# Kernel optimization log

Measured on AMD Instinct MI355X. Metric: run time of the kernel, lower is better.

The kernel has to match this reference:

```python
import jax, jax.numpy as jnp
import numpy as np
from jax import lax

H = 64  # hidden_size

def _lstm_layer(x, w_ih, w_hh, b_ih, b_hh):
    # x: (B, T, in). PyTorch gate order [i, f, g, o]; gates = x@W_ih^T + h@W_hh^T + b_ih + b_hh.
    B, T, _ = x.shape
    xw = jnp.einsum('bti,gi->btg', x, w_ih) + (b_ih + b_hh)  # (B, T, 4H), input projection hoisted out of scan

    def step(carry, xw_t):
        h, c = carry
        gates = xw_t + h @ w_hh.T                     # (B, 4H)
        i, f, g, o = jnp.split(gates, 4, axis=-1)
        i = jax.nn.sigmoid(i)
        f = jax.nn.sigmoid(f)
        g = jnp.tanh(g)
        o = jax.nn.sigmoid(o)
        c = f * c + i * g
        h = o * jnp.tanh(c)
        return (h, c), h

    h0 = jnp.zeros((B, H), dtype=x.dtype)
    c0 = jnp.zeros((B, H), dtype=x.dtype)
    (h_n, _), hs = lax.scan(step, (h0, c0), jnp.swapaxes(xw, 0, 1))  # hs: (T, B, H)
    return jnp.swapaxes(hs, 0, 1), h_n


def setup_inputs() -> dict:
    key = jax.random.key(0)
    ks = jax.random.split(key, 12)
    s = 1.0 / np.sqrt(H)  # PyTorch LSTM init scale
    return {
        'x':     jax.random.normal(ks[0], (2048, 512, 4), dtype=jnp.float32),
        'w_ih0': jax.random.uniform(ks[1], (4 * H, 4), jnp.float32, -s, s),
        'w_hh0': jax.random.uniform(ks[2], (4 * H, H), jnp.float32, -s, s),
        'b_ih0': jax.random.uniform(ks[3], (4 * H,), jnp.float32, -s, s),
        'b_hh0': jax.random.uniform(ks[4], (4 * H,), jnp.float32, -s, s),
        'w_ih1': jax.random.uniform(ks[5], (4 * H, H), jnp.float32, -s, s),
        'w_hh1': jax.random.uniform(ks[6], (4 * H, H), jnp.float32, -s, s),
        'b_ih1': jax.random.uniform(ks[7], (4 * H,), jnp.float32, -s, s),
        'b_hh1': jax.random.uniform(ks[8], (4 * H,), jnp.float32, -s, s),
        'fc_w':  jax.random.uniform(ks[9], (H, H), jnp.float32, -s, s),
        'fc_b':  jax.random.uniform(ks[10], (H,), jnp.float32, -s, s),
    }


def reference(x, w_ih0, w_hh0, b_ih0, b_hh0, w_ih1, w_hh1, b_ih1, b_hh1, fc_w, fc_b):
    # 2-layer LSTM (eval mode: inter-layer dropout inactive), take last layer's final hidden,
    # then Linear + tanh.
    h1_seq, _ = _lstm_layer(x, w_ih0, w_hh0, b_ih0, b_hh0)
    _, h_n = _lstm_layer(h1_seq, w_ih1, w_hh1, b_ih1, b_hh1)
    return jnp.tanh(h_n @ fc_w.T + fc_b)
```

## Files before the change

### kernel.cpp

```cpp
#include <hip/hip_runtime.h>


#define HID 64
#define TSTEPS 512
#define MB 8
#define BLK 512
#define HSTR 88
#define LOG2E  1.4426950408889634f
#define LOG2E2 2.8853900817779268f

typedef _Float16 f16;
typedef _Float16 half8 __attribute__((ext_vector_type(8)));
typedef _Float16 half4 __attribute__((ext_vector_type(4)));
typedef float f32x4 __attribute__((ext_vector_type(4)));

__device__ __forceinline__ float tanh2(float y) {
    return fmaf(2.0f, __builtin_amdgcn_rcpf(1.0f + __builtin_amdgcn_exp2f(-y)), -1.0f);
}

__global__ __launch_bounds__(BLK, 2) void lstm_mfma(
    const float* __restrict__ x,
    const float* __restrict__ w_ih0,
    const float* __restrict__ w_hh0,
    const float* __restrict__ b_ih0,
    const float* __restrict__ b_hh0,
    const float* __restrict__ w_ih1,
    const float* __restrict__ w_hh1,
    const float* __restrict__ b_ih1,
    const float* __restrict__ b_hh1,
    const float* __restrict__ fc_w,
    const float* __restrict__ fc_b,
    float* __restrict__ out)
{
    __shared__ f16 xs[TSTEPS * MB * 4];
    __shared__ f16 h0s[2][MB * HSTR];
    __shared__ f16 h1s[2][MB * HSTR];

    const int tid  = threadIdx.x;
    const int w    = tid >> 6;
    const int l    = tid & 63;
    const int quad = l >> 4;
    const int l15  = l & 15;
    const int wl   = w & 3;
    const bool isL0 = (w < 4);
    const int b0   = blockIdx.x * MB;

    const int RM = (l15 < 8) ? l15 : ((l15 & 4) | ((l15 + 2) & 3));

    for (int it = tid; it < MB * TSTEPS; it += BLK) {
        const int m = it >> 9;
        const int t = it & 511;
        const float4 v = *((const float4*)x + (size_t)(b0 + m) * TSTEPS + t);
        *(half4*)(xs + (t * MB + m) * 4) =
            (half4){ (f16)v.x, (f16)v.y, (f16)v.z, (f16)v.w };
    }
    for (int it = tid; it < MB * HSTR; it += BLK) {
        h0s[0][it] = (f16)0.f; h0s[1][it] = (f16)0.f;
        h1s[0][it] = (f16)0.f; h1s[1][it] = (f16)0.f;
    }

    half8 Bf[4][4];
    f32x4 biasv[4];
    const half8 Z = { (f16)0.f,(f16)0.f,(f16)0.f,(f16)0.f,
                      (f16)0.f,(f16)0.f,(f16)0.f,(f16)0.f };
    #pragma unroll
    for (int ti = 0; ti < 4; ++ti) {
        const int n = (wl + 4 * ti) * 16 + l15;
        const float sc = (ti == 2) ? LOG2E2 : LOG2E;
        float bval;
        if (isL0) {
            bval = (b_ih0[n] + b_hh0[n]) * sc;
            half8 pz = Z;
            if (quad == 0) {
                const float4 v = *(const float4*)(w_ih0 + n * 4);
                pz[0] = (f16)(v.x * sc); pz[1] = (f16)(v.y * sc);
                pz[2] = (f16)(v.z * sc); pz[3] = (f16)(v.w * sc);
            }
            Bf[ti][0] = pz;
            #pragma unroll
            for (int ks = 0; ks < 2; ++ks) {
                const int ko = ks * 32 + quad * 8;
                const float4 a = *(const float4*)(w_hh0 + n * HID + ko);
                const float4 b = *(const float4*)(w_hh0 + n * HID + ko + 4);
                Bf[ti][1 + ks] = (half8){
                    (f16)(a.x*sc),(f16)(a.y*sc),(f16)(a.z*sc),(f16)(a.w*sc),
                    (f16)(b.x*sc),(f16)(b.y*sc),(f16)(b.z*sc),(f16)(b.w*sc) };
            }
            Bf[ti][3] = Z;
        } else {
            bval = (b_ih1[n] + b_hh1[n]) * sc;
            #pragma unroll
            for (int ks = 0; ks < 2; ++ks) {
                const int ko = ks * 32 + quad * 8;
                const float4 a = *(const float4*)(w_ih1 + n * HID + ko);
                const float4 b = *(const float4*)(w_ih1 + n * HID + ko + 4);
                Bf[ti][ks] = (half8){
                    (f16)(a.x*sc),(f16)(a.y*sc),(f16)(a.z*sc),(f16)(a.w*sc),
                    (f16)(b.x*sc),(f16)(b.y*sc),(f16)(b.z*sc),(f16)(b.w*sc) };
                const float4 c = *(const float4*)(w_hh1 + n * HID + ko);
                const float4 d = *(const float4*)(w_hh1 + n * HID + ko + 4);
                Bf[ti][2 + ks] = (half8){
                    (f16)(c.x*sc),(f16)(c.y*sc),(f16)(c.z*sc),(f16)(c.w*sc),
                    (f16)(d.x*sc),(f16)(d.y*sc),(f16)(d.z*sc),(f16)(d.w*sc) };
            }
        }
        biasv[ti] = (f32x4){ bval, bval, bval, bval };
    }

    const int  mrow = (quad & 1) * 4 + (quad & 2);
    const int  uu   = wl * 16 + l15;
    const int  hb   = RM * HSTR + quad * 8;
    float cst0 = 0.f, cst1 = 0.f;
    f32x4 g[4];

    auto load_x = [&](int r) -> half4 {
        return *(const half4*)(xs + (r * MB + RM) * 4);
    };
    auto l0_mfma = [&](half4 xv, const f16* h0rd) {
        const half8 A1 = *(const half8*)(h0rd + hb);
        const half8 A2 = *(const half8*)(h0rd + hb + 32);
        half8 ax = Z;
        if (quad == 0) { ax[0]=xv[0]; ax[1]=xv[1]; ax[2]=xv[2]; ax[3]=xv[3]; }
        f32x4 acc[4];
        #pragma unroll
        for (int ti = 0; ti < 4; ++ti)
            acc[ti] = __builtin_amdgcn_mfma_f32_16x16x32_f16(ax, Bf[ti][0], biasv[ti], 0, 0, 0);
        #pragma unroll
        for (int ti = 0; ti < 4; ++ti)
            acc[ti] = __builtin_amdgcn_mfma_f32_16x16x32_f16(A1, Bf[ti][1], acc[ti], 0, 0, 0);
        #pragma unroll
        for (int ti = 0; ti < 4; ++ti)
            g[ti]   = __builtin_amdgcn_mfma_f32_16x16x32_f16(A2, Bf[ti][2], acc[ti], 0, 0, 0);
    };
    auto l1_mfma = [&](const f16* h0rd, const f16* h1rd) {
        const half8 A1 = *(const half8*)(h0rd + hb);
        const half8 A2 = *(const half8*)(h0rd + hb + 32);
        const half8 A3 = *(const half8*)(h1rd + hb);
        const half8 A4 = *(const half8*)(h1rd + hb + 32);
        f32x4 acc[4];
        #pragma unroll
        for (int ti = 0; ti < 4; ++ti)
            acc[ti] = __builtin_amdgcn_mfma_f32_16x16x32_f16(A1, Bf[ti][0], biasv[ti], 0, 0, 0);
        #pragma unroll
        for (int ti = 0; ti < 4; ++ti)
            acc[ti] = __builtin_amdgcn_mfma_f32_16x16x32_f16(A2, Bf[ti][1], acc[ti], 0, 0, 0);
        #pragma unroll
        for (int ti = 0; ti < 4; ++ti)
            acc[ti] = __builtin_amdgcn_mfma_f32_16x16x32_f16(A3, Bf[ti][2], acc[ti], 0, 0, 0);
        #pragma unroll
        for (int ti = 0; ti < 4; ++ti)
            g[ti]   = __builtin_amdgcn_mfma_f32_16x16x32_f16(A4, Bf[ti][3], acc[ti], 0, 0, 0);
    };
    auto act_store = [&](f16* dst) {
        #pragma unroll
        for (int j = 0; j < 2; ++j) {
            const float ei = __builtin_amdgcn_exp2f(-g[0][j]);
            const float ef = __builtin_amdgcn_exp2f(-g[1][j]);
            const float eg = __builtin_amdgcn_exp2f(-g[2][j]);
            const float eo = __builtin_amdgcn_exp2f(-g[3][j]);
            float& c = j ? cst1 : cst0;
            const float af = 1.0f + ef;
            const float P  = (1.0f + ei) * (1.0f + eg);
            c = fmaf(c, P, (1.0f - eg) * af) * __builtin_amdgcn_rcpf(P * af);
            const float ym = fminf(-LOG2E2 * c, 126.0f);
            const float ec = __builtin_amdgcn_exp2f(ym);
            const float r2 = __builtin_amdgcn_rcpf((1.0f + eo) * (1.0f + ec));
            dst[(mrow + j) * HSTR + uu] = (f16)((1.0f - ec) * r2);
        }
    };

    __syncthreads();

    half4 xv;
    if (isL0) xv = load_x(0);
    if (isL0) { l0_mfma(xv, h0s[1]); act_store(h0s[0]); xv = load_x(1); }
    __syncthreads();
    if (isL0) { l0_mfma(xv, h0s[0]); act_store(h0s[1]); xv = load_x(2); }
    else      { l1_mfma(h0s[0], h1s[1]); act_store(h1s[0]); }
    __syncthreads();

    #pragma unroll 1
    for (int r = 2; r < 510; r += 2) {
        if (isL0) { l0_mfma(xv, h0s[1]); act_store(h0s[0]); xv = load_x(r + 1); }
        else      { l1_mfma(h0s[1], h1s[0]); act_store(h1s[1]); }
        __syncthreads();
        if (isL0) { l0_mfma(xv, h0s[0]); act_store(h0s[1]); xv = load_x(r + 2); }
        else      { l1_mfma(h0s[0], h1s[1]); act_store(h1s[0]); }
        __syncthreads();
    }
    if (isL0) { l0_mfma(xv, h0s[1]); act_store(h0s[0]); xv = load_x(511); }
    else      { l1_mfma(h0s[1], h1s[0]); act_store(h1s[1]); }
    __syncthreads();
    if (isL0) { l0_mfma(xv, h0s[0]); act_store(h0s[1]); }
    else      { l1_mfma(h0s[0], h1s[1]); act_store(h1s[0]); }
    __syncthreads();
    if (!isL0) { l1_mfma(h0s[1], h1s[0]); act_store(h1s[1]); }
    __syncthreads();

    {
        const int v = tid & 63;
        const int m = tid >> 6;
        float a = fc_b[v];
        const f16* hp = h1s[1] + m * HSTR;
        const float4* wp = (const float4*)(fc_w + v * HID);
        #pragma unroll
        for (int kk = 0; kk < HID / 4; ++kk) {
            const float4 wv = wp[kk];
            a += (float)hp[kk * 4 + 0] * wv.x + (float)hp[kk * 4 + 1] * wv.y
               + (float)hp[kk * 4 + 2] * wv.z + (float)hp[kk * 4 + 3] * wv.w;
        }
        out[(size_t)(b0 + m) * HID + v] = tanh2(a * LOG2E2);
    }
}

extern "C" void kernel_launch(void* const* d_in, const int* in_sizes, int n_in,
                              void* d_out, int out_size, void* d_ws, size_t ws_size,
                              hipStream_t stream) {
    const float* x     = (const float*)d_in[0];
    const float* w_ih0 = (const float*)d_in[1];
    const float* w_hh0 = (const float*)d_in[2];
    const float* b_ih0 = (const float*)d_in[3];
    const float* b_hh0 = (const float*)d_in[4];
    const float* w_ih1 = (const float*)d_in[5];
    const float* w_hh1 = (const float*)d_in[6];
    const float* b_ih1 = (const float*)d_in[7];
    const float* b_hh1 = (const float*)d_in[8];
    const float* fc_w  = (const float*)d_in[9];
    const float* fc_b  = (const float*)d_in[10];
    float* out = (float*)d_out;

    const int B = in_sizes[0] / (TSTEPS * 4);
    lstm_mfma<<<dim3(B / MB), dim3(BLK), 0, stream>>>(
        x, w_ih0, w_hh0, b_ih0, b_hh0, w_ih1, w_hh1, b_ih1, b_hh1, fc_w, fc_b, out);
}
```

Baseline: 330.2 us.

## Interleave layer waves and stagger MFMA and activation phases across half-steps

Layer-0 and layer-1 waves are now interleaved (even/odd waves) rather than split into the first and second halves of the block. Each timestep is split into an MFMA phase and an activation phase, so one layer's matrix work runs while the other layer does its transcendental activations, with a barrier between phases. Layer 1's hidden state becomes single-buffered, and the x load is clamped at the final timestep. The aim is to overlap MFMA and VALU work across waves on the same SIMD, at the cost of twice as many __syncthreads per step.

After: 397.8 us. +20.5%, slower.

```diff
diff --git a/kernel.cpp b/kernel.cpp
--- a/kernel.cpp
+++ b/kernel.cpp
@@ -34,15 +34,15 @@
 {
     __shared__ f16 xs[TSTEPS * MB * 4];
     __shared__ f16 h0s[2][MB * HSTR];
-    __shared__ f16 h1s[2][MB * HSTR];
+    __shared__ f16 h1s[MB * HSTR];
 
     const int tid  = threadIdx.x;
     const int w    = tid >> 6;
     const int l    = tid & 63;
     const int quad = l >> 4;
     const int l15  = l & 15;
-    const int wl   = w & 3;
-    const bool isL0 = (w < 4);
+    const int wl   = w >> 1;
+    const bool isL0 = ((w & 1) == 0);
     const int b0   = blockIdx.x * MB;
 
     const int RM = (l15 < 8) ? l15 : ((l15 & 4) | ((l15 + 2) & 3));
@@ -55,8 +55,7 @@
             (half4){ (f16)v.x, (f16)v.y, (f16)v.z, (f16)v.w };
     }
     for (int it = tid; it < MB * HSTR; it += BLK) {
-        h0s[0][it] = (f16)0.f; h0s[1][it] = (f16)0.f;
-        h1s[0][it] = (f16)0.f; h1s[1][it] = (f16)0.f;
+        h0s[0][it] = (f16)0.f; h0s[1][it] = (f16)0.f; h1s[it] = (f16)0.f;
     }
 
     half8 Bf[4][4];
@@ -114,7 +113,8 @@
     f32x4 g[4];
 
     auto load_x = [&](int r) -> half4 {
-        return *(const half4*)(xs + (r * MB + RM) * 4);
+        const int t = (r < TSTEPS) ? r : (TSTEPS - 1);
+        return *(const half4*)(xs + (t * MB + RM) * 4);
     };
     auto l0_mfma = [&](half4 xv, const f16* h0rd) {
         const half8 A1 = *(const half8*)(h0rd + hb);
@@ -132,11 +132,11 @@
         for (int ti = 0; ti < 4; ++ti)
             g[ti]   = __builtin_amdgcn_mfma_f32_16x16x32_f16(A2, Bf[ti][2], acc[ti], 0, 0, 0);
     };
-    auto l1_mfma = [&](const f16* h0rd, const f16* h1rd) {
+    auto l1_mfma = [&](const f16* h0rd) {
         const half8 A1 = *(const half8*)(h0rd + hb);
         const half8 A2 = *(const half8*)(h0rd + hb + 32);
-        const half8 A3 = *(const half8*)(h1rd + hb);
-        const half8 A4 = *(const half8*)(h1rd + hb + 32);
+        const half8 A3 = *(const half8*)(h1s + hb);
+        const half8 A4 = *(const half8*)(h1s + hb + 32);
         f32x4 acc[4];
         #pragma unroll
         for (int ti = 0; ti < 4; ++ti)
@@ -173,35 +173,44 @@
 
     half4 xv;
     if (isL0) xv = load_x(0);
-    if (isL0) { l0_mfma(xv, h0s[1]); act_store(h0s[0]); xv = load_x(1); }
-    __syncthreads();
-    if (isL0) { l0_mfma(xv, h0s[0]); act_store(h0s[1]); xv = load_x(2); }
-    else      { l1_mfma(h0s[0], h1s[1]); act_store(h1s[0]); }
+    if (isL0) l0_mfma(xv, h0s[1]);
+    __syncthreads();
+    if (isL0) { act_store(h0s[0]); xv = load_x(1); }
+    __syncthreads();
+    if (isL0) l0_mfma(xv, h0s[0]);
+    __syncthreads();
+    if (isL0) { act_store(h0s[1]); xv = load_x(2); }
+    else      l1_mfma(h0s[0]);
     __syncthreads();
 
     #pragma unroll 1
-    for (int r = 2; r < 510; r += 2) {
-        if (isL0) { l0_mfma(xv, h0s[1]); act_store(h0s[0]); xv = load_x(r + 1); }
-        else      { l1_mfma(h0s[1], h1s[0]); act_store(h1s[1]); }
-        __syncthreads();
-        if (isL0) { l0_mfma(xv, h0s[0]); act_store(h0s[1]); xv = load_x(r + 2); }
-        else      { l1_mfma(h0s[0], h1s[1]); act_store(h1s[0]); }
-        __syncthreads();
-    }
-    if (isL0) { l0_mfma(xv, h0s[1]); act_store(h0s[0]); xv = load_x(511); }
-    else      { l1_mfma(h0s[1], h1s[0]); act_store(h1s[1]); }
-    __syncthreads();
-    if (isL0) { l0_mfma(xv, h0s[0]); act_store(h0s[1]); }
-    else      { l1_mfma(h0s[0], h1s[1]); act_store(h1s[0]); }
-    __syncthreads();
-    if (!isL0) { l1_mfma(h0s[1], h1s[0]); act_store(h1s[1]); }
+    for (int r = 2; r < TSTEPS; r += 2) {
+        if (isL0) l0_mfma(xv, h0s[1]);
+        else      act_store(h1s);
+        __syncthreads();
+        if (isL0) { act_store(h0s[0]); xv = load_x(r + 1); }
+        else      l1_mfma(h0s[1]);
+        __syncthreads();
+        if (isL0) l0_mfma(xv, h0s[0]);
+        else      act_store(h1s);
+        __syncthreads();
+        if (isL0) { act_store(h0s[1]); xv = load_x(r + 2); }
+        else      l1_mfma(h0s[0]);
+        __syncthreads();
+    }
+
+    if (!isL0) act_store(h1s);
+    __syncthreads();
+    if (!isL0) l1_mfma(h0s[1]);
+    __syncthreads();
+    if (!isL0) act_store(h1s);
     __syncthreads();
 
     {
         const int v = tid & 63;
         const int m = tid >> 6;
         float a = fc_b[v];
-        const f16* hp = h1s[1] + m * HSTR;
+        const f16* hp = h1s + m * HSTR;
         const float4* wp = (const float4*)(fc_w + v * HID);
         #pragma unroll
         for (int kk = 0; kk < HID / 4; ++kk) {
```
